# Optimization experiments

Measured on AMD Instinct MI355X. Metric: run time of the kernel, lower is better.

The kernel has to match this reference:

```python
import jax, jax.numpy as jnp
import numpy as np

TEMPERATURE = 8.0  # sqrt(head_dim=64)
NEG = -1e9


def setup_inputs() -> dict:
    key = jax.random.key(0)
    kq, kk, kv = jax.random.split(key, 3)
    B, H, S, D = 2, 16, 2048, 64
    q = jax.random.normal(kq, (B, H, S, D), dtype=jnp.float32)
    k = jax.random.normal(kk, (B, H, S, D), dtype=jnp.float32)
    v = jax.random.normal(kv, (B, H, S, D), dtype=jnp.float32)
    attn_mask = jnp.ones((B, 1, 1, S), dtype=jnp.int32)  # 1 = keep, 0 = mask
    return {"q": q, "k": k, "v": v, "attn_mask": attn_mask}


def reference(q, k, v, attn_mask):
    # attn = (q / T) @ k^T  -> [B,H,S,S]
    scores = jnp.einsum('bhqd,bhkd->bhqk', q / TEMPERATURE, k)
    # optional padding mask: fill where mask == 0
    scores = jnp.where(attn_mask == 0, NEG, scores)
    # causal mask: triu(diagonal=1) positions are masked (key index > query index)
    S = scores.shape[-1]
    row = jnp.arange(S)[:, None]
    col = jnp.arange(S)[None, :]
    scores = jnp.where(col > row, NEG, scores)
    attn = jax.nn.softmax(scores, axis=-1)
    out = jnp.einsum('bhqk,bhkd->bhqd', attn, v)
    return (out, attn)
```

## Files before the change

### kernel.cpp

```cpp
#include <hip/hip_runtime.h>

#define NEG (-1e9f)

typedef __attribute__((ext_vector_type(8))) short bf16x8;
typedef __attribute__((ext_vector_type(4))) float f32x4;

static constexpr int Ss = 2048, Dd = 64;

__device__ __forceinline__ unsigned short f2bf(float f) {
  union { float f; unsigned u; } v; v.f = f;
  unsigned r = v.u + 0x7FFF + ((v.u >> 16) & 1);
  return (unsigned short)(r >> 16);
}

__global__ __launch_bounds__(256) void prep_kernel(
    const float* __restrict__ k, const float* __restrict__ v,
    unsigned short* __restrict__ kbf, unsigned short* __restrict__ vtbf) {
  const int tid = threadIdx.x;
  const int bh = blockIdx.x >> 5;
  const int st = blockIdx.x & 31;
  __shared__ unsigned short Vl[64 * 68];
  const size_t base = ((size_t)bh * Ss + (size_t)st * 64) * Dd;
#pragma unroll
  for (int i = 0; i < 4; ++i) {
    int idx4 = tid + i * 256;
    int row = idx4 >> 4, col = (idx4 & 15) * 4;
    float4 f = *(const float4*)(k + base + row * 64 + col);
    ushort4 u;
    u.x = f2bf(f.x); u.y = f2bf(f.y); u.z = f2bf(f.z); u.w = f2bf(f.w);
    *(ushort4*)&kbf[base + row * 64 + col] = u;
    float4 g = *(const float4*)(v + base + row * 64 + col);
    ushort4 w;
    w.x = f2bf(g.x); w.y = f2bf(g.y); w.z = f2bf(g.z); w.w = f2bf(g.w);
    *(ushort4*)&Vl[row * 68 + col] = w;
  }
  __syncthreads();
  const int d = tid >> 2, sb = (tid & 3) * 16;
  bf16x8 a, b;
#pragma unroll
  for (int i = 0; i < 8; ++i) a[i] = (short)Vl[(sb + i) * 68 + d];
#pragma unroll
  for (int i = 0; i < 8; ++i) b[i] = (short)Vl[(sb + 8 + i) * 68 + d];
  unsigned short* vo = vtbf + ((size_t)bh * Dd + d) * Ss + (size_t)st * 64 + sb;
  *(bf16x8*)vo = a;
  *(bf16x8*)(vo + 8) = b;
}

__global__ __launch_bounds__(256) void attn_kernel(
    const float* __restrict__ q, const unsigned short* __restrict__ kbf,
    const unsigned short* __restrict__ vtbf, const int* __restrict__ mask,
    float* __restrict__ out, float* __restrict__ attn) {
  const int tid = threadIdx.x;
  const int wave = tid >> 6, lane = tid & 63, quad = lane >> 4, ln15 = lane & 15;
  const int bh = blockIdx.x & 31;
  const int qt = 31 - (blockIdx.x >> 5);
  const int b = bh >> 4;
  const int qloc = wave * 16 + ln15;
  const int qg = qt * 64 + qloc;

  __shared__ unsigned short Plds[64 * 72];

  bf16x8 qf0, qf1;
  {
    const float* qp = q + ((size_t)bh * Ss + qg) * Dd + quad * 8;
    float4 f0 = *(const float4*)(qp);
    float4 f1 = *(const float4*)(qp + 4);
    float4 f2 = *(const float4*)(qp + 32);
    float4 f3 = *(const float4*)(qp + 36);
    qf0[0] = (short)f2bf(f0.x * 0.125f); qf0[1] = (short)f2bf(f0.y * 0.125f);
    qf0[2] = (short)f2bf(f0.z * 0.125f); qf0[3] = (short)f2bf(f0.w * 0.125f);
    qf0[4] = (short)f2bf(f1.x * 0.125f); qf0[5] = (short)f2bf(f1.y * 0.125f);
    qf0[6] = (short)f2bf(f1.z * 0.125f); qf0[7] = (short)f2bf(f1.w * 0.125f);
    qf1[0] = (short)f2bf(f2.x * 0.125f); qf1[1] = (short)f2bf(f2.y * 0.125f);
    qf1[2] = (short)f2bf(f2.z * 0.125f); qf1[3] = (short)f2bf(f2.w * 0.125f);
    qf1[4] = (short)f2bf(f3.x * 0.125f); qf1[5] = (short)f2bf(f3.y * 0.125f);
    qf1[6] = (short)f2bf(f3.z * 0.125f); qf1[7] = (short)f2bf(f3.w * 0.125f);
  }

  const unsigned short* kb = kbf + (size_t)bh * Ss * Dd;
  const unsigned short* vb = vtbf + (size_t)bh * Dd * Ss;
  const int* mrowp = mask + (size_t)b * Ss;

  float m = -1e30f, l = 0.0f;

  for (int j = 0; j <= qt; ++j) {
    unsigned long long mm = __ballot(mrowp[j * 64 + lane] != 0);
    float sv[16];
#pragma unroll
    for (int c = 0; c < 4; ++c) {
      const unsigned short* kr = kb + (size_t)(j * 64 + c * 16 + ln15) * Dd + quad * 8;
      bf16x8 kf0 = *(const bf16x8*)(kr);
      bf16x8 kf1 = *(const bf16x8*)(kr + 32);
      f32x4 acc = {0.f, 0.f, 0.f, 0.f};
      acc = __builtin_amdgcn_mfma_f32_16x16x32_bf16(kf0, qf0, acc, 0, 0, 0);
      acc = __builtin_amdgcn_mfma_f32_16x16x32_bf16(kf1, qf1, acc, 0, 0, 0);
#pragma unroll
      for (int r = 0; r < 4; ++r) sv[c * 4 + r] = acc[r];
    }
    if (j == qt || mm != ~0ull) {
#pragma unroll
      for (int c = 0; c < 4; ++c)
#pragma unroll
        for (int r = 0; r < 4; ++r) {
          int kl = c * 16 + quad * 4 + r;
          bool mz = !((mm >> kl) & 1);
          if (j * 64 + kl > qg || mz) sv[c * 4 + r] = NEG;
        }
    }
    float t0 = fmaxf(fmaxf(sv[0], sv[1]), fmaxf(sv[2], sv[3]));
    float t1 = fmaxf(fmaxf(sv[4], sv[5]), fmaxf(sv[6], sv[7]));
    float t2 = fmaxf(fmaxf(sv[8], sv[9]), fmaxf(sv[10], sv[11]));
    float t3 = fmaxf(fmaxf(sv[12], sv[13]), fmaxf(sv[14], sv[15]));
    float tm = fmaxf(fmaxf(t0, t1), fmaxf(t2, t3));
    tm = fmaxf(tm, __shfl_xor(tm, 16));
    tm = fmaxf(tm, __shfl_xor(tm, 32));
    float mnew = fmaxf(m, tm);
    float ss = 0.f;
#pragma unroll
    for (int i = 0; i < 16; ++i) ss += __expf(sv[i] - mnew);
    ss += __shfl_xor(ss, 16);
    ss += __shfl_xor(ss, 32);
    l = l * __expf(m - mnew) + ss;
    m = mnew;
  }

  const float rl = 1.0f / l;
  f32x4 oacc[4];
#pragma unroll
  for (int c = 0; c < 4; ++c) oacc[c] = (f32x4){0.f, 0.f, 0.f, 0.f};

  float* arow = attn + ((size_t)bh * Ss + qg) * Ss;

  for (int j = 0; j < 32; ++j) {
    if (j <= qt) {
      unsigned long long mm = __ballot(mrowp[j * 64 + lane] != 0);
      float sv[16];
#pragma unroll
      for (int c = 0; c < 4; ++c) {
        const unsigned short* kr = kb + (size_t)(j * 64 + c * 16 + ln15) * Dd + quad * 8;
        bf16x8 kf0 = *(const bf16x8*)(kr);
        bf16x8 kf1 = *(const bf16x8*)(kr + 32);
        f32x4 acc = {0.f, 0.f, 0.f, 0.f};
        acc = __builtin_amdgcn_mfma_f32_16x16x32_bf16(kf0, qf0, acc, 0, 0, 0);
        acc = __builtin_amdgcn_mfma_f32_16x16x32_bf16(kf1, qf1, acc, 0, 0, 0);
#pragma unroll
        for (int r = 0; r < 4; ++r) sv[c * 4 + r] = acc[r];
      }
      if (j == qt || mm != ~0ull) {
#pragma unroll
        for (int c = 0; c < 4; ++c)
#pragma unroll
          for (int r = 0; r < 4; ++r) {
            int kl = c * 16 + quad * 4 + r;
            bool mz = !((mm >> kl) & 1);
            if (j * 64 + kl > qg || mz) sv[c * 4 + r] = NEG;
          }
      }
#pragma unroll
      for (int c = 0; c < 4; ++c) {
        float4 pv;
        pv.x = __expf(sv[c * 4 + 0] - m) * rl;
        pv.y = __expf(sv[c * 4 + 1] - m) * rl;
        pv.z = __expf(sv[c * 4 + 2] - m) * rl;
        pv.w = __expf(sv[c * 4 + 3] - m) * rl;
        *(float4*)&arow[j * 64 + c * 16 + quad * 4] = pv;
        ushort4 u;
        u.x = f2bf(pv.x); u.y = f2bf(pv.y); u.z = f2bf(pv.z); u.w = f2bf(pv.w);
        *(ushort4*)&Plds[qloc * 72 + c * 16 + quad * 4] = u;
      }
#pragma unroll
      for (int ch = 0; ch < 2; ++ch) {
        bf16x8 pf = *(const bf16x8*)&Plds[qloc * 72 + quad * 8 + 32 * ch];
#pragma unroll
        for (int c = 0; c < 4; ++c) {
          bf16x8 vf = *(const bf16x8*)&vb[(size_t)(c * 16 + ln15) * Ss + j * 64 + quad * 8 + 32 * ch];
          oacc[c] = __builtin_amdgcn_mfma_f32_16x16x32_bf16(vf, pf, oacc[c], 0, 0, 0);
        }
      }
    } else {
      float4 z = {0.f, 0.f, 0.f, 0.f};
#pragma unroll
      for (int i = 0; i < 4; ++i) {
        int idx4 = tid + i * 256;
        int row = idx4 >> 4, col = (idx4 & 15) * 4;
        *(float4*)&attn[((size_t)bh * Ss + qt * 64 + row) * Ss + j * 64 + col] = z;
      }
    }
  }

#pragma unroll
  for (int c = 0; c < 4; ++c)
    *(f32x4*)&out[((size_t)bh * Ss + qg) * Dd + c * 16 + quad * 4] = oacc[c];
}

__global__ __launch_bounds__(256) void attn_kernel_fb(
    const float* __restrict__ q, const float* __restrict__ k,
    const float* __restrict__ v, const int* __restrict__ mask,
    float* __restrict__ out, float* __restrict__ attn) {
  const int tid  = threadIdx.x;
  const int wave = tid >> 6;
  const int lane = tid & 63;
  const int quad = lane >> 4;
  const int ln15 = lane & 15;

  const int bh = blockIdx.x & 31;
  const int qt = 31 - (blockIdx.x >> 5);
  const int b  = bh >> 4;

  __shared__ unsigned short Klds[64 * 72];
  __shared__ unsigned short Vlds[64 * 72];
  __shared__ unsigned short Plds[64 * 72];

  {
    const float* qp = q + ((size_t)bh * Ss + (size_t)qt * 64) * Dd;
#pragma unroll
    for (int i = 0; i < 4; ++i) {
      int idx4 = tid + i * 256;
      int row = idx4 >> 4, col = (idx4 & 15) * 4;
      float4 f = *(const float4*)(qp + row * 64 + col);
      ushort4 u;
      u.x = f2bf(f.x * 0.125f); u.y = f2bf(f.y * 0.125f);
      u.z = f2bf(f.z * 0.125f); u.w = f2bf(f.w * 0.125f);
      *(ushort4*)&Vlds[row * 72 + col] = u;
    }
  }
  __syncthreads();
  const bf16x8 qfrag0 = *(const bf16x8*)&Vlds[(wave * 16 + ln15) * 72 + quad * 8];
  const bf16x8 qfrag1 = *(const bf16x8*)&Vlds[(wave * 16 + ln15) * 72 + quad * 8 + 32];

  float mrow[4], lrow[4];
#pragma unroll
  for (int r = 0; r < 4; ++r) { mrow[r] = -1e30f; lrow[r] = 0.0f; }

  for (int j = 0; j <= qt; ++j) {
    __syncthreads();
    {
      const float* kp = k + ((size_t)bh * Ss + (size_t)j * 64) * Dd;
#pragma unroll
      for (int i = 0; i < 4; ++i) {
        int idx4 = tid + i * 256;
        int row = idx4 >> 4, col = (idx4 & 15) * 4;
        float4 f = *(const float4*)(kp + row * 64 + col);
        ushort4 u;
        u.x = f2bf(f.x); u.y = f2bf(f.y); u.z = f2bf(f.z); u.w = f2bf(f.w);
        *(ushort4*)&Klds[row * 72 + col] = u;
      }
    }
    __syncthreads();
    unsigned long long mm = __ballot(mask[(size_t)b * Ss + j * 64 + lane] != 0);

    float sv[4][4];
#pragma unroll
    for (int c = 0; c < 4; ++c) {
      bf16x8 kf0 = *(const bf16x8*)&Klds[(c * 16 + ln15) * 72 + quad * 8];
      bf16x8 kf1 = *(const bf16x8*)&Klds[(c * 16 + ln15) * 72 + quad * 8 + 32];
      f32x4 acc = {0.f, 0.f, 0.f, 0.f};
      acc = __builtin_amdgcn_mfma_f32_16x16x32_bf16(qfrag0, kf0, acc, 0, 0, 0);
      acc = __builtin_amdgcn_mfma_f32_16x16x32_bf16(qfrag1, kf1, acc, 0, 0, 0);
      int col = j * 64 + c * 16 + ln15;
      bool mz = !((mm >> (c * 16 + ln15)) & 1);
#pragma unroll
      for (int r = 0; r < 4; ++r) {
        int row = qt * 64 + wave * 16 + quad * 4 + r;
        float val = acc[r];
        if (col > row || mz) val = NEG;
        sv[c][r] = val;
      }
    }
#pragma unroll
    for (int r = 0; r < 4; ++r) {
      float tm = fmaxf(fmaxf(sv[0][r], sv[1][r]), fmaxf(sv[2][r], sv[3][r]));
      tm = fmaxf(tm, __shfl_xor(tm, 1));
      tm = fmaxf(tm, __shfl_xor(tm, 2));
      tm = fmaxf(tm, __shfl_xor(tm, 4));
      tm = fmaxf(tm, __shfl_xor(tm, 8));
      float mnew = fmaxf(mrow[r], tm);
      float ss = __expf(sv[0][r] - mnew) + __expf(sv[1][r] - mnew) +
                 __expf(sv[2][r] - mnew) + __expf(sv[3][r] - mnew);
      ss += __shfl_xor(ss, 1);
      ss += __shfl_xor(ss, 2);
      ss += __shfl_xor(ss, 4);
      ss += __shfl_xor(ss, 8);
      lrow[r] = lrow[r] * __expf(mrow[r] - mnew) + ss;
      mrow[r] = mnew;
    }
  }

  float rl4[4];
#pragma unroll
  for (int r = 0; r < 4; ++r) rl4[r] = 1.0f / lrow[r];

  f32x4 oacc[4];
#pragma unroll
  for (int c = 0; c < 4; ++c) oacc[c] = (f32x4){0.f, 0.f, 0.f, 0.f};

  for (int j = 0; j < 32; ++j) {
    if (j <= qt) {
      __syncthreads();
      {
        const float* kp = k + ((size_t)bh * Ss + (size_t)j * 64) * Dd;
        const float* vp = v + ((size_t)bh * Ss + (size_t)j * 64) * Dd;
#pragma unroll
        for (int i = 0; i < 4; ++i) {
          int idx4 = tid + i * 256;
          int row = idx4 >> 4, col = (idx4 & 15) * 4;
          float4 f = *(const float4*)(kp + row * 64 + col);
          ushort4 u;
          u.x = f2bf(f.x); u.y = f2bf(f.y); u.z = f2bf(f.z); u.w = f2bf(f.w);
          *(ushort4*)&Klds[row * 72 + col] = u;
          float4 g = *(const float4*)(vp + row * 64 + col);
          ushort4 w2;
          w2.x = f2bf(g.x); w2.y = f2bf(g.y); w2.z = f2bf(g.z); w2.w = f2bf(g.w);
          *(ushort4*)&Vlds[row * 72 + col] = w2;
        }
      }
      __syncthreads();
      unsigned long long mm = __ballot(mask[(size_t)b * Ss + j * 64 + lane] != 0);
#pragma unroll
      for (int c = 0; c < 4; ++c) {
        bf16x8 kf0 = *(const bf16x8*)&Klds[(c * 16 + ln15) * 72 + quad * 8];
        bf16x8 kf1 = *(const bf16x8*)&Klds[(c * 16 + ln15) * 72 + quad * 8 + 32];
        f32x4 acc = {0.f, 0.f, 0.f, 0.f};
        acc = __builtin_amdgcn_mfma_f32_16x16x32_bf16(qfrag0, kf0, acc, 0, 0, 0);
        acc = __builtin_amdgcn_mfma_f32_16x16x32_bf16(qfrag1, kf1, acc, 0, 0, 0);
        int col = j * 64 + c * 16 + ln15;
        bool mz = !((mm >> (c * 16 + ln15)) & 1);
#pragma unroll
        for (int r = 0; r < 4; ++r) {
          int row = qt * 64 + wave * 16 + quad * 4 + r;
          float val = acc[r];
          if (col > row || mz) val = NEG;
          float p = __expf(val - mrow[r]) * rl4[r];
          attn[((size_t)bh * Ss + row) * Ss + col] = p;
          Plds[(wave * 16 + quad * 4 + r) * 72 + c * 16 + ln15] = f2bf(p);
        }
      }
#pragma unroll
      for (int ch = 0; ch < 2; ++ch) {
        bf16x8 pf = *(const bf16x8*)&Plds[(wave * 16 + ln15) * 72 + quad * 8 + 32 * ch];
#pragma unroll
        for (int c = 0; c < 4; ++c) {
          bf16x8 vf;
#pragma unroll
          for (int jj = 0; jj < 8; ++jj)
            vf[jj] = (short)Vlds[(quad * 8 + jj + 32 * ch) * 72 + c * 16 + ln15];
          oacc[c] = __builtin_amdgcn_mfma_f32_16x16x32_bf16(pf, vf, oacc[c], 0, 0, 0);
        }
      }
    } else {
      float4 z = {0.f, 0.f, 0.f, 0.f};
#pragma unroll
      for (int i = 0; i < 4; ++i) {
        int idx4 = tid + i * 256;
        int row = idx4 >> 4, col = (idx4 & 15) * 4;
        *(float4*)&attn[((size_t)bh * Ss + qt * 64 + row) * Ss + j * 64 + col] = z;
      }
    }
  }

#pragma unroll
  for (int c = 0; c < 4; ++c)
#pragma unroll
    for (int r = 0; r < 4; ++r) {
      int row = qt * 64 + wave * 16 + quad * 4 + r;
      out[((size_t)bh * Ss + row) * Dd + c * 16 + ln15] = oacc[c][r];
    }
}

extern "C" void kernel_launch(void* const* d_in, const int* in_sizes, int n_in,
                              void* d_out, int out_size, void* d_ws, size_t ws_size,
                              hipStream_t stream) {
  const float* q    = (const float*)d_in[0];
  const float* k    = (const float*)d_in[1];
  const float* v    = (const float*)d_in[2];
  const int*   mask = (const int*)d_in[3];
  float* out  = (float*)d_out;
  float* attn = out + (size_t)2 * 16 * 2048 * 64;

  const size_t need = (size_t)2 * 32 * Ss * Dd * sizeof(unsigned short);
  if (d_ws != nullptr && ws_size >= need) {
    unsigned short* kbf  = (unsigned short*)d_ws;
    unsigned short* vtbf = kbf + (size_t)32 * Ss * Dd;
    prep_kernel<<<dim3(32 * 32), dim3(256), 0, stream>>>(k, v, kbf, vtbf);
    attn_kernel<<<dim3(32 * 32), dim3(256), 0, stream>>>(q, kbf, vtbf, mask, out, attn);
  } else {
    attn_kernel_fb<<<dim3(32 * 32), dim3(256), 0, stream>>>(q, k, v, mask, out, attn);
  }
}
```

Measured before the change: 769.3 us.

## Pre-swizzle K/V tiles into MFMA fragment order and double-buffer via direct global-to-LDS loads

The prep kernel now writes K and V^T in a per-tile layout that matches the MFMA fragment order, so each wave reads 16-byte contiguous chunks. The attention kernel stages K and V tiles into double-buffered shared memory with global_load_lds, prefetching the next tile while computing the current one, and synchronises each iteration. It also reorders query-tile scheduling to interleave short and long causal tiles, XOR-swizzles the P tile in LDS, and moves the zero-fill of masked tiles into a separate loop. The aim is to hide global K/V load latency and balance work across blocks, at the cost of extra block-wide barriers and more LDS.

```diff
diff --git a/kernel.cpp b/kernel.cpp
--- a/kernel.cpp
+++ b/kernel.cpp
@@ -12,15 +12,24 @@
   unsigned r = v.u + 0x7FFF + ((v.u >> 16) & 1);
   return (unsigned short)(r >> 16);
 }
+
+__device__ __forceinline__ void gl_lds16(const unsigned short* g, unsigned short* l) {
+  __builtin_amdgcn_global_load_lds(
+      (const __attribute__((address_space(1))) unsigned int*)g,
+      (__attribute__((address_space(3))) unsigned int*)l, 16, 0, 0);
+}
+
+#define PIDX(row, col) ((((row) * 64) + (col)) ^ (((row) & 7) << 3))
 
 __global__ __launch_bounds__(256) void prep_kernel(
     const float* __restrict__ k, const float* __restrict__ v,
     unsigned short* __restrict__ kbf, unsigned short* __restrict__ vtbf) {
   const int tid = threadIdx.x;
   const int bh = blockIdx.x >> 5;
-  const int st = blockIdx.x & 31;
-  __shared__ unsigned short Vl[64 * 68];
-  const size_t base = ((size_t)bh * Ss + (size_t)st * 64) * Dd;
+  const int j  = blockIdx.x & 31;
+  __shared__ __align__(16) unsigned short Kl[64 * 72];
+  __shared__ __align__(16) unsigned short Vl[64 * 72];
+  const size_t base = ((size_t)bh * Ss + (size_t)j * 64) * Dd;
 #pragma unroll
   for (int i = 0; i < 4; ++i) {
     int idx4 = tid + i * 256;
@@ -28,22 +37,33 @@
     float4 f = *(const float4*)(k + base + row * 64 + col);
     ushort4 u;
     u.x = f2bf(f.x); u.y = f2bf(f.y); u.z = f2bf(f.z); u.w = f2bf(f.w);
-    *(ushort4*)&kbf[base + row * 64 + col] = u;
+    *(ushort4*)&Kl[row * 72 + col] = u;
     float4 g = *(const float4*)(v + base + row * 64 + col);
     ushort4 w;
     w.x = f2bf(g.x); w.y = f2bf(g.y); w.z = f2bf(g.z); w.w = f2bf(g.w);
-    *(ushort4*)&Vl[row * 68 + col] = w;
+    *(ushort4*)&Vl[row * 72 + col] = w;
   }
   __syncthreads();
-  const int d = tid >> 2, sb = (tid & 3) * 16;
-  bf16x8 a, b;
-#pragma unroll
-  for (int i = 0; i < 8; ++i) a[i] = (short)Vl[(sb + i) * 68 + d];
-#pragma unroll
-  for (int i = 0; i < 8; ++i) b[i] = (short)Vl[(sb + 8 + i) * 68 + d];
-  unsigned short* vo = vtbf + ((size_t)bh * Dd + d) * Ss + (size_t)st * 64 + sb;
-  *(bf16x8*)vo = a;
-  *(bf16x8*)(vo + 8) = b;
+  const size_t tb = ((size_t)bh * 32 + j) * 4096;
+#pragma unroll
+  for (int t = 0; t < 2; ++t) {
+    int id = tid + t * 256;
+    int ck = id >> 6, ln = id & 63;
+    int c = ck >> 1, ph = ck & 1;
+    bf16x8 val = *(const bf16x8*)&Kl[(c * 16 + (ln & 15)) * 72 + (ln >> 4) * 8 + ph * 32];
+    *(bf16x8*)&kbf[tb + ck * 512 + ln * 8] = val;
+  }
+#pragma unroll
+  for (int t = 0; t < 2; ++t) {
+    int id = tid + t * 256;
+    int ck = id >> 6, ln = id & 63;
+    int c = ck >> 1, ch = ck & 1;
+    bf16x8 val;
+#pragma unroll
+    for (int i = 0; i < 8; ++i)
+      val[i] = (short)Vl[(ch * 32 + (ln >> 4) * 8 + i) * 72 + c * 16 + (ln & 15)];
+    *(bf16x8*)&vtbf[tb + ck * 512 + ln * 8] = val;
+  }
 }
 
 __global__ __launch_bounds__(256) void attn_kernel(
@@ -53,12 +73,15 @@
   const int tid = threadIdx.x;
   const int wave = tid >> 6, lane = tid & 63, quad = lane >> 4, ln15 = lane & 15;
   const int bh = blockIdx.x & 31;
-  const int qt = 31 - (blockIdx.x >> 5);
+  const int g = blockIdx.x >> 5, h = g & 7, kk = g >> 3;
+  const int qt = (kk < 2) ? (h * 2 + kk) : (31 - h * 2 - (kk & 1));
   const int b = bh >> 4;
   const int qloc = wave * 16 + ln15;
   const int qg = qt * 64 + qloc;
 
-  __shared__ unsigned short Plds[64 * 72];
+  __shared__ __align__(16) unsigned short Kb[2 * 4096];
+  __shared__ __align__(16) unsigned short Vb[2 * 4096];
+  __shared__ __align__(16) unsigned short Plds[4096];
 
   bf16x8 qf0, qf1;
   {
@@ -77,20 +100,29 @@
     qf1[6] = (short)f2bf(f3.z * 0.125f); qf1[7] = (short)f2bf(f3.w * 0.125f);
   }
 
-  const unsigned short* kb = kbf + (size_t)bh * Ss * Dd;
-  const unsigned short* vb = vtbf + (size_t)bh * Dd * Ss;
+  const unsigned short* kt = kbf + ((size_t)bh * 32) * 4096;
+  const unsigned short* vt = vtbf + ((size_t)bh * 32) * 4096;
   const int* mrowp = mask + (size_t)b * Ss;
+  const int c0 = wave * 2, c1 = wave * 2 + 1;
 
   float m = -1e30f, l = 0.0f;
 
+  gl_lds16(kt + c0 * 512 + lane * 8, &Kb[c0 * 512]);
+  gl_lds16(kt + c1 * 512 + lane * 8, &Kb[c1 * 512]);
+  __syncthreads();
   for (int j = 0; j <= qt; ++j) {
+    const int cur = j & 1;
+    if (j < qt) {
+      const unsigned short* nt = kt + (size_t)(j + 1) * 4096;
+      gl_lds16(nt + c0 * 512 + lane * 8, &Kb[(cur ^ 1) * 4096 + c0 * 512]);
+      gl_lds16(nt + c1 * 512 + lane * 8, &Kb[(cur ^ 1) * 4096 + c1 * 512]);
+    }
     unsigned long long mm = __ballot(mrowp[j * 64 + lane] != 0);
     float sv[16];
 #pragma unroll
     for (int c = 0; c < 4; ++c) {
-      const unsigned short* kr = kb + (size_t)(j * 64 + c * 16 + ln15) * Dd + quad * 8;
-      bf16x8 kf0 = *(const bf16x8*)(kr);
-      bf16x8 kf1 = *(const bf16x8*)(kr + 32);
+      bf16x8 kf0 = *(const bf16x8*)&Kb[cur * 4096 + (c * 2 + 0) * 512 + lane * 8];
+      bf16x8 kf1 = *(const bf16x8*)&Kb[cur * 4096 + (c * 2 + 1) * 512 + lane * 8];
       f32x4 acc = {0.f, 0.f, 0.f, 0.f};
       acc = __builtin_amdgcn_mfma_f32_16x16x32_bf16(kf0, qf0, acc, 0, 0, 0);
       acc = __builtin_amdgcn_mfma_f32_16x16x32_bf16(kf1, qf1, acc, 0, 0, 0);
@@ -122,69 +154,83 @@
     ss += __shfl_xor(ss, 32);
     l = l * __expf(m - mnew) + ss;
     m = mnew;
+    __syncthreads();
   }
 
   const float rl = 1.0f / l;
   f32x4 oacc[4];
 #pragma unroll
   for (int c = 0; c < 4; ++c) oacc[c] = (f32x4){0.f, 0.f, 0.f, 0.f};
-
   float* arow = attn + ((size_t)bh * Ss + qg) * Ss;
 
-  for (int j = 0; j < 32; ++j) {
-    if (j <= qt) {
-      unsigned long long mm = __ballot(mrowp[j * 64 + lane] != 0);
-      float sv[16];
+  gl_lds16(kt + c0 * 512 + lane * 8, &Kb[c0 * 512]);
+  gl_lds16(kt + c1 * 512 + lane * 8, &Kb[c1 * 512]);
+  gl_lds16(vt + c0 * 512 + lane * 8, &Vb[c0 * 512]);
+  gl_lds16(vt + c1 * 512 + lane * 8, &Vb[c1 * 512]);
+  __syncthreads();
+  for (int j = 0; j <= qt; ++j) {
+    const int cur = j & 1;
+    if (j < qt) {
+      const unsigned short* ntk = kt + (size_t)(j + 1) * 4096;
+      const unsigned short* ntv = vt + (size_t)(j + 1) * 4096;
+      gl_lds16(ntk + c0 * 512 + lane * 8, &Kb[(cur ^ 1) * 4096 + c0 * 512]);
+      gl_lds16(ntk + c1 * 512 + lane * 8, &Kb[(cur ^ 1) * 4096 + c1 * 512]);
+      gl_lds16(ntv + c0 * 512 + lane * 8, &Vb[(cur ^ 1) * 4096 + c0 * 512]);
+      gl_lds16(ntv + c1 * 512 + lane * 8, &Vb[(cur ^ 1) * 4096 + c1 * 512]);
+    }
+    unsigned long long mm = __ballot(mrowp[j * 64 + lane] != 0);
+    float sv[16];
+#pragma unroll
+    for (int c = 0; c < 4; ++c) {
+      bf16x8 kf0 = *(const bf16x8*)&Kb[cur * 4096 + (c * 2 + 0) * 512 + lane * 8];
+      bf16x8 kf1 = *(const bf16x8*)&Kb[cur * 4096 + (c * 2 + 1) * 512 + lane * 8];
+      f32x4 acc = {0.f, 0.f, 0.f, 0.f};
+      acc = __builtin_amdgcn_mfma_f32_16x16x32_bf16(kf0, qf0, acc, 0, 0, 0);
+      acc = __builtin_amdgcn_mfma_f32_16x16x32_bf16(kf1, qf1, acc, 0, 0, 0);
+#pragma unroll
+      for (int r = 0; r < 4; ++r) sv[c * 4 + r] = acc[r];
+    }
+    if (j == qt || mm != ~0ull) {
+#pragma unroll
+      for (int c = 0; c < 4; ++c)
+#pragma unroll
+        for (int r = 0; r < 4; ++r) {
+          int kl = c * 16 + quad * 4 + r;
+          bool mz = !((mm >> kl) & 1);
+          if (j * 64 + kl > qg || mz) sv[c * 4 + r] = NEG;
+        }
+    }
+#pragma unroll
+    for (int c = 0; c < 4; ++c) {
+      float4 pv;
+      pv.x = __expf(sv[c * 4 + 0] - m) * rl;
+      pv.y = __expf(sv[c * 4 + 1] - m) * rl;
+      pv.z = __expf(sv[c * 4 + 2] - m) * rl;
+      pv.w = __expf(sv[c * 4 + 3] - m) * rl;
+      *(float4*)&arow[j * 64 + c * 16 + quad * 4] = pv;
+      ushort4 u;
+      u.x = f2bf(pv.x); u.y = f2bf(pv.y); u.z = f2bf(pv.z); u.w = f2bf(pv.w);
+      *(ushort4*)&Plds[PIDX(qloc, c * 16 + quad * 4)] = u;
+    }
+#pragma unroll
+    for (int ch = 0; ch < 2; ++ch) {
+      bf16x8 pf = *(const bf16x8*)&Plds[PIDX(qloc, quad * 8 + 32 * ch)];
 #pragma unroll
       for (int c = 0; c < 4; ++c) {
-        const unsigned short* kr = kb + (size_t)(j * 64 + c * 16 + ln15) * Dd + quad * 8;
-        bf16x8 kf0 = *(const bf16x8*)(kr);
-        bf16x8 kf1 = *(const bf16x8*)(kr + 32);
-        f32x4 acc = {0.f, 0.f, 0.f, 0.f};
-        acc = __builtin_amdgcn_mfma_f32_16x16x32_bf16(kf0, qf0, acc, 0, 0, 0);
-        acc = __builtin_amdgcn_mfma_f32_16x16x32_bf16(kf1, qf1, acc, 0, 0, 0);
-#pragma unroll
-        for (int r = 0; r < 4; ++r) sv[c * 4 + r] = acc[r];
-      }
-      if (j == qt || mm != ~0ull) {
-#pragma unroll
-        for (int c = 0; c < 4; ++c)
-#pragma unroll
-          for (int r = 0; r < 4; ++r) {
-            int kl = c * 16 + quad * 4 + r;
-            bool mz = !((mm >> kl) & 1);
-            if (j * 64 + kl > qg || mz) sv[c * 4 + r] = NEG;
-          }
-      }
-#pragma unroll
-      for (int c = 0; c < 4; ++c) {
-        float4 pv;
-        pv.x = __expf(sv[c * 4 + 0] - m) * rl;
-        pv.y = __expf(sv[c * 4 + 1] - m) * rl;
-        pv.z = __expf(sv[c * 4 + 2] - m) * rl;
-        pv.w = __expf(sv[c * 4 + 3] - m) * rl;
-        *(float4*)&arow[j * 64 + c * 16 + quad * 4] = pv;
-        ushort4 u;
-        u.x = f2bf(pv.x); u.y = f2bf(pv.y); u.z = f2bf(pv.z); u.w = f2bf(pv.w);
-        *(ushort4*)&Plds[qloc * 72 + c * 16 + quad * 4] = u;
-      }
-#pragma unroll
-      for (int ch = 0; ch < 2; ++ch) {
-        bf16x8 pf = *(const bf16x8*)&Plds[qloc * 72 + quad * 8 + 32 * ch];
-#pragma unroll
-        for (int c = 0; c < 4; ++c) {
-          bf16x8 vf = *(const bf16x8*)&vb[(size_t)(c * 16 + ln15) * Ss + j * 64 + quad * 8 + 32 * ch];
-          oacc[c] = __builtin_amdgcn_mfma_f32_16x16x32_bf16(vf, pf, oacc[c], 0, 0, 0);
-        }
-      }
-    } else {
-      float4 z = {0.f, 0.f, 0.f, 0.f};
-#pragma unroll
-      for (int i = 0; i < 4; ++i) {
-        int idx4 = tid + i * 256;
-        int row = idx4 >> 4, col = (idx4 & 15) * 4;
-        *(float4*)&attn[((size_t)bh * Ss + qt * 64 + row) * Ss + j * 64 + col] = z;
-      }
+        bf16x8 vf = *(const bf16x8*)&Vb[cur * 4096 + (c * 2 + ch) * 512 + lane * 8];
+        oacc[c] = __builtin_amdgcn_mfma_f32_16x16x32_bf16(vf, pf, oacc[c], 0, 0, 0);
+      }
+    }
+    __syncthreads();
+  }
+
+  for (int j = qt + 1; j < 32; ++j) {
+    float4 z = {0.f, 0.f, 0.f, 0.f};
+#pragma unroll
+    for (int i = 0; i < 4; ++i) {
+      int idx4 = tid + i * 256;
+      int row = idx4 >> 4, col = (idx4 & 15) * 4;
+      *(float4*)&attn[((size_t)bh * Ss + qt * 64 + row) * Ss + j * 64 + col] = z;
     }
   }
 
@@ -209,7 +255,7 @@
 
   __shared__ unsigned short Klds[64 * 72];
   __shared__ unsigned short Vlds[64 * 72];
-  __shared__ unsigned short Plds[64 * 72];
+  __shared__ unsigned short Plds2[64 * 72];
 
   {
     const float* qp = q + ((size_t)bh * Ss + (size_t)qt * 64) * Dd;
@@ -332,12 +378,12 @@
           if (col > row || mz) val = NEG;
           float p = __expf(val - mrow[r]) * rl4[r];
           attn[((size_t)bh * Ss + row) * Ss + col] = p;
-          Plds[(wave * 16 + quad * 4 + r) * 72 + c * 16 + ln15] = f2bf(p);
+          Plds2[(wave * 16 + quad * 4 + r) * 72 + c * 16 + ln15] = f2bf(p);
         }
       }
 #pragma unroll
       for (int ch = 0; ch < 2; ++ch) {
-        bf16x8 pf = *(const bf16x8*)&Plds[(wave * 16 + ln15) * 72 + quad * 8 + 32 * ch];
+        bf16x8 pf = *(const bf16x8*)&Plds2[(wave * 16 + ln15) * 72 + quad * 8 + 32 * ch];
 #pragma unroll
         for (int c = 0; c < 4; ++c) {
           bf16x8 vf;
```

After: 646.7 us. -15.9%, faster.
